# Kernel optimization log

Measured on AMD Instinct MI355X. Metric: run time of the kernel, lower is better.

## Reference

```python
import jax, jax.numpy as jnp
import numpy as np

F = 128
E = 100000   # num_edges
T = 1000000  # num_triplets


def setup_inputs() -> dict:
    key = jax.random.key(0)
    ks = jax.random.split(key, 20)
    s = 0.05
    return {
        "f": jax.random.normal(ks[0], (E, 2 * F), jnp.float32),
        "M01": jax.random.normal(ks[1], (T, F), jnp.float32),
        "M02": jax.random.normal(ks[2], (T, F), jnp.float32),
        # split_net MLP([2F, 2F, 2F]): Linear -> act -> Linear
        "W1": jax.random.normal(ks[3], (2 * F, 2 * F), jnp.float32) * s,
        "b1": jnp.zeros((2 * F,), jnp.float32),
        "W2": jax.random.normal(ks[4], (2 * F, 2 * F), jnp.float32) * s,
        "b2": jnp.zeros((2 * F,), jnp.float32),
        "Ws01": jax.random.normal(ks[5], (F, F), jnp.float32) * s,
        "bs01": jnp.zeros((F,), jnp.float32),
        "Ws02": jax.random.normal(ks[6], (F, F), jnp.float32) * s,
        "bs02": jnp.zeros((F,), jnp.float32),
        "Ws": jax.random.normal(ks[7], (2 * F, F), jnp.float32) * s,
        "bs": jnp.zeros((F,), jnp.float32),
        "Wout": jax.random.normal(ks[8], (F, F), jnp.float32) * s,
        "bout": jnp.zeros((F,), jnp.float32),
        "num_edges": E,
        "idx_ji": jax.random.randint(ks[9], (T,), 0, E, jnp.int32),
        "idx_ki": jax.random.randint(ks[10], (T,), 0, E, jnp.int32),
    }


def reference(f, M01, M02, W1, b1, W2, b2, Ws01, bs01, Ws02, bs02, Ws, bs,
              Wout, bout, num_edges, idx_ji, idx_ki):
    act = jax.nn.silu
    # f = act(split_net(f)); split_net = Linear -> act -> Linear
    h = act(act(f @ W1 + b1) @ W2 + b2)          # [E, 2F]
    f01, f02 = jnp.split(h, 2, axis=-1)           # [E, F] each
    # triplet interaction: gather -> multiply -> linear -> act
    s01 = act((f01[idx_ki] * M01 * f01[idx_ji]) @ Ws01 + bs01)  # [T, F]
    s02 = act((f02[idx_ki] * M02 * f02[idx_ji]) @ Ws02 + bs02)  # [T, F]
    s = act(jnp.concatenate((s01, s02), axis=-1) @ Ws + bs)     # [T, F]
    # scatter-sum triplets back to edges
    out = jax.ops.segment_sum(s, idx_ji, num_segments=num_edges)  # [E, F]
    return out @ Wout + bout
```

## Files before the change

kernel.cpp:

```cpp
#include <hip/hip_runtime.h>

typedef __attribute__((ext_vector_type(8))) short short8;
typedef __attribute__((ext_vector_type(4))) float f32x4;

__device__ __forceinline__ float silu_f(float x) { return x / (1.0f + __expf(-x)); }

__device__ __forceinline__ unsigned short f2bf(float x) {
  unsigned u = __float_as_uint(x);
  u += 0x7FFFu + ((u >> 16) & 1u);
  return (unsigned short)(u >> 16);
}
__device__ __forceinline__ float bf2f(unsigned short v) {
  return __uint_as_float(((unsigned)v) << 16);
}
__device__ __forceinline__ unsigned cvtpk_bf16(float lo, float hi) {
  unsigned r;
  asm("v_cvt_pk_bf16_f32 %0, %1, %2" : "=v"(r) : "v"(lo), "v"(hi));
  return r;
}

#define TSYNC() do { asm volatile("s_waitcnt lgkmcnt(0)" ::: "memory"); \
                     __builtin_amdgcn_s_barrier(); \
                     asm volatile("" ::: "memory"); } while (0)

__global__ void prep_w(const float* __restrict__ W, unsigned short* __restrict__ wh,
                       unsigned short* __restrict__ wl, int K, int N)
{
  int e = blockIdx.x * 256 + threadIdx.x;
  if (e >= K * N) return;
  int k = e / N, n = e % N;
  float w = W[e];
  unsigned short hi = f2bf(w);
  unsigned short lo = f2bf(w - bf2f(hi));
  int kp = k >> 6, kk = k & 63;
  size_t dst = (size_t)kp * N * 64 + (size_t)n * 64 + ((((kk >> 3) ^ (n & 7)) << 3)) + (kk & 7);
  wh[dst] = hi;
  wl[dst] = lo;
}

template<int INBF, int ASPLIT>
__global__ __launch_bounds__(512)
void mlp_gemm(const void* A_, const unsigned short* __restrict__ wh,
              const unsigned short* __restrict__ wl,
              const float* __restrict__ bias, unsigned short* __restrict__ C, int M)
{
  __shared__ unsigned short aTh[64 * 64], aTl[64 * 64];
  __shared__ unsigned short whb[256 * 64], wlb[256 * 64];
  const int tid = threadIdx.x;
  const int lane = tid & 63, wv = tid >> 6;
  const int g = wv & 3, hh = wv >> 2;
  const int l15 = lane & 15, l4 = lane >> 4;
  const int row0 = blockIdx.x * 64;
  const int r = tid >> 3, kseg = (tid & 7) * 8;
  const f32x4 zero4 = {0.f, 0.f, 0.f, 0.f};

  f32x4 acc[8];
#pragma unroll
  for (int nt = 0; nt < 8; nt++) acc[nt] = zero4;

  for (int kp = 0; kp < 4; kp++) {
    {
      const int grow = row0 + r;
      float x[8];
      if (grow < M) {
        if (INBF) {
          short8 v = *(const short8*)((const unsigned short*)A_ + (size_t)grow * 256 + kp * 64 + kseg);
#pragma unroll
          for (int j = 0; j < 8; j++) x[j] = bf2f((unsigned short)v[j]);
        } else {
          const float* ap = (const float*)A_ + (size_t)grow * 256 + kp * 64 + kseg;
          float4 v0 = *(const float4*)ap;
          float4 v1 = *(const float4*)(ap + 4);
          x[0] = v0.x; x[1] = v0.y; x[2] = v0.z; x[3] = v0.w;
          x[4] = v1.x; x[5] = v1.y; x[6] = v1.z; x[7] = v1.w;
        }
      } else {
#pragma unroll
        for (int j = 0; j < 8; j++) x[j] = 0.f;
      }
      union { short8 s; unsigned short us[8]; } H, L;
#pragma unroll
      for (int j = 0; j < 8; j++) {
        H.us[j] = f2bf(x[j]);
        L.us[j] = ASPLIT ? f2bf(x[j] - bf2f(H.us[j])) : (unsigned short)0;
      }
      const int dst = r * 64 + ((((kseg >> 3) ^ (r & 7)) << 3));
      *(short8*)(aTh + dst) = H.s;
      if (ASPLIT) *(short8*)(aTl + dst) = L.s;
    }
    {
      const short8* srcH = (const short8*)(wh + (size_t)kp * 16384);
      const short8* srcL = (const short8*)(wl + (size_t)kp * 16384);
#pragma unroll
      for (int i = 0; i < 4; i++) {
        ((short8*)whb)[tid + 512 * i] = srcH[tid + 512 * i];
        ((short8*)wlb)[tid + 512 * i] = srcL[tid + 512 * i];
      }
    }
    __syncthreads();
#pragma unroll
    for (int ks = 0; ks < 2; ks++) {
      const int arow = 16 * g + l15;
      const int aof = arow * 64 + (((4 * ks + l4) ^ (arow & 7)) << 3);
      short8 ah = *(const short8*)(aTh + aof);
      short8 al = *(const short8*)(aTl + aof);
#pragma unroll
      for (int nt = 0; nt < 8; nt++) {
        const int col = 128 * hh + 16 * nt + l15;
        const int bof = col * 64 + (((4 * ks + l4) ^ (col & 7)) << 3);
        short8 bh = *(const short8*)(whb + bof);
        short8 bl = *(const short8*)(wlb + bof);
        acc[nt] = __builtin_amdgcn_mfma_f32_16x16x32_bf16(ah, bh, acc[nt], 0, 0, 0);
        acc[nt] = __builtin_amdgcn_mfma_f32_16x16x32_bf16(ah, bl, acc[nt], 0, 0, 0);
        if (ASPLIT)
          acc[nt] = __builtin_amdgcn_mfma_f32_16x16x32_bf16(al, bh, acc[nt], 0, 0, 0);
      }
    }
    __syncthreads();
  }
#pragma unroll
  for (int nt = 0; nt < 8; nt++) {
    const int col = 128 * hh + 16 * nt + l15;
    const float bv = bias[col];
#pragma unroll
    for (int i = 0; i < 4; i++) {
      const int row = row0 + 16 * g + 4 * l4 + i;
      if (row < M) C[(size_t)row * 256 + col] = f2bf(silu_f(acc[nt][i] + bv));
    }
  }
}

__global__ __launch_bounds__(512)
void final_gemm(const float* __restrict__ A, const unsigned short* __restrict__ wh,
                const unsigned short* __restrict__ wl,
                const float* __restrict__ bias, float* __restrict__ C, int M)
{
  __shared__ unsigned short aTh[64 * 64], aTl[64 * 64];
  __shared__ unsigned short whb[128 * 64], wlb[128 * 64];
  const int tid = threadIdx.x;
  const int lane = tid & 63, wv = tid >> 6;
  const int g = wv & 3, hh = wv >> 2;
  const int l15 = lane & 15, l4 = lane >> 4;
  const int row0 = blockIdx.x * 64;
  const int r = tid >> 3, kseg = (tid & 7) * 8;
  const f32x4 zero4 = {0.f, 0.f, 0.f, 0.f};

  f32x4 acc[4];
#pragma unroll
  for (int nt = 0; nt < 4; nt++) acc[nt] = zero4;

  for (int kp = 0; kp < 2; kp++) {
    {
      const int grow = row0 + r;
      float x[8];
      if (grow < M) {
        const float* ap = A + (size_t)grow * 128 + kp * 64 + kseg;
        float4 v0 = *(const float4*)ap;
        float4 v1 = *(const float4*)(ap + 4);
        x[0] = v0.x; x[1] = v0.y; x[2] = v0.z; x[3] = v0.w;
        x[4] = v1.x; x[5] = v1.y; x[6] = v1.z; x[7] = v1.w;
      } else {
#pragma unroll
        for (int j = 0; j < 8; j++) x[j] = 0.f;
      }
      union { short8 s; unsigned short us[8]; } H, L;
#pragma unroll
      for (int j = 0; j < 8; j++) {
        H.us[j] = f2bf(x[j]);
        L.us[j] = f2bf(x[j] - bf2f(H.us[j]));
      }
      const int dst = r * 64 + ((((kseg >> 3) ^ (r & 7)) << 3));
      *(short8*)(aTh + dst) = H.s;
      *(short8*)(aTl + dst) = L.s;
    }
    {
      const short8* srcH = (const short8*)(wh + (size_t)kp * 8192);
      const short8* srcL = (const short8*)(wl + (size_t)kp * 8192);
#pragma unroll
      for (int i = 0; i < 2; i++) {
        ((short8*)whb)[tid + 512 * i] = srcH[tid + 512 * i];
        ((short8*)wlb)[tid + 512 * i] = srcL[tid + 512 * i];
      }
    }
    __syncthreads();
#pragma unroll
    for (int ks = 0; ks < 2; ks++) {
      const int arow = 16 * g + l15;
      const int aof = arow * 64 + (((4 * ks + l4) ^ (arow & 7)) << 3);
      short8 ah = *(const short8*)(aTh + aof);
      short8 al = *(const short8*)(aTl + aof);
#pragma unroll
      for (int nt = 0; nt < 4; nt++) {
        const int col = 64 * hh + 16 * nt + l15;
        const int bof = col * 64 + (((4 * ks + l4) ^ (col & 7)) << 3);
        short8 bh = *(const short8*)(whb + bof);
        short8 bl = *(const short8*)(wlb + bof);
        acc[nt] = __builtin_amdgcn_mfma_f32_16x16x32_bf16(ah, bh, acc[nt], 0, 0, 0);
        acc[nt] = __builtin_amdgcn_mfma_f32_16x16x32_bf16(ah, bl, acc[nt], 0, 0, 0);
        acc[nt] = __builtin_amdgcn_mfma_f32_16x16x32_bf16(al, bh, acc[nt], 0, 0, 0);
      }
    }
    __syncthreads();
  }
#pragma unroll
  for (int nt = 0; nt < 4; nt++) {
    const int col = 64 * hh + 16 * nt + l15;
    const float bv = bias[col];
#pragma unroll
    for (int i = 0; i < 4; i++) {
      const int row = row0 + 16 * g + 4 * l4 + i;
      if (row < M) C[(size_t)row * 128 + col] = acc[nt][i] + bv;
    }
  }
}

__global__ void hist_k(const int* __restrict__ ji, int* __restrict__ cnt, int T) {
  int t = blockIdx.x * 256 + threadIdx.x;
  const int stride = gridDim.x * 256;
  for (; t < T; t += stride) atomicAdd(&cnt[ji[t]], 1);
}

__global__ void scan1_k(const int* __restrict__ cnt, int* __restrict__ csum, int E) {
  __shared__ int red[256];
  const int c0 = blockIdx.x * 2048;
  int s = 0;
  for (int i = threadIdx.x; i < 2048; i += 256) {
    int e = c0 + i;
    if (e < E) s += cnt[e];
  }
  red[threadIdx.x] = s;
  __syncthreads();
  for (int o = 128; o > 0; o >>= 1) {
    if (threadIdx.x < o) red[threadIdx.x] += red[threadIdx.x + o];
    __syncthreads();
  }
  if (threadIdx.x == 0) csum[blockIdx.x] = red[0];
}

__global__ void scan2_k(int* __restrict__ csum, int n) {
  if (threadIdx.x == 0 && blockIdx.x == 0) {
    int acc = 0;
    for (int i = 0; i < n; i++) { int v = csum[i]; csum[i] = acc; acc += v; }
  }
}

__global__ void scan3_k(const int* __restrict__ cnt, const int* __restrict__ csum,
                        int* __restrict__ off, int E) {
  __shared__ int ts[256];
  const int c0 = blockIdx.x * 2048;
  const int tid = threadIdx.x;
  int loc[8];
  int s = 0;
#pragma unroll
  for (int k = 0; k < 8; k++) {
    int e = c0 + tid * 8 + k;
    loc[k] = (e < E) ? cnt[e] : 0;
    s += loc[k];
  }
  ts[tid] = s;
  __syncthreads();
  for (int o = 1; o < 256; o <<= 1) {
    int v = (tid >= o) ? ts[tid - o] : 0;
    __syncthreads();
    ts[tid] += v;
    __syncthreads();
  }
  int base = csum[blockIdx.x] + ((tid > 0) ? ts[tid - 1] : 0);
#pragma unroll
  for (int k = 0; k < 8; k++) {
    int e = c0 + tid * 8 + k;
    if (e < E) { off[e] = base; base += loc[k]; }
  }
}

__global__ void scatter_k(const int* __restrict__ ji, int* __restrict__ cursor,
                          int* __restrict__ perm, int T) {
  int t = blockIdx.x * 256 + threadIdx.x;
  const int stride = gridDim.x * 256;
  for (; t < T; t += stride) {
    int e = ji[t];
    int p = atomicAdd(&cursor[e], 1);
    perm[p] = t;
  }
}

struct G12 {
  short8 a0, a1;
  short8 b0, b1;
  float4 m0, m1, m2, m3;
};

__device__ __forceinline__ void issue12(G12& g, const unsigned short* __restrict__ fa,
                                        const unsigned short* __restrict__ fb,
                                        const float* __restrict__ mm, int cseg)
{
  g.a0 = *(const short8*)(fa + cseg);
  g.a1 = *(const short8*)(fa + cseg + 8);
  g.b0 = *(const short8*)(fb + cseg);
  g.b1 = *(const short8*)(fb + cseg + 8);
  g.m0 = *(const float4*)(mm + cseg + 0);
  g.m1 = *(const float4*)(mm + cseg + 4);
  g.m2 = *(const float4*)(mm + cseg + 8);
  g.m3 = *(const float4*)(mm + cseg + 12);
}

__device__ __forceinline__ void pack8x(const short8& a, const short8& b,
                                       const float4& m0, const float4& m1, short8& o)
{
  float p[8];
  p[0] = bf2f((unsigned short)a[0]) * m0.x * bf2f((unsigned short)b[0]);
  p[1] = bf2f((unsigned short)a[1]) * m0.y * bf2f((unsigned short)b[1]);
  p[2] = bf2f((unsigned short)a[2]) * m0.z * bf2f((unsigned short)b[2]);
  p[3] = bf2f((unsigned short)a[3]) * m0.w * bf2f((unsigned short)b[3]);
  p[4] = bf2f((unsigned short)a[4]) * m1.x * bf2f((unsigned short)b[4]);
  p[5] = bf2f((unsigned short)a[5]) * m1.y * bf2f((unsigned short)b[5]);
  p[6] = bf2f((unsigned short)a[6]) * m1.z * bf2f((unsigned short)b[6]);
  p[7] = bf2f((unsigned short)a[7]) * m1.w * bf2f((unsigned short)b[7]);
  union { short8 s; unsigned u[4]; } t;
  t.u[0] = cvtpk_bf16(p[0], p[1]);
  t.u[1] = cvtpk_bf16(p[2], p[3]);
  t.u[2] = cvtpk_bf16(p[4], p[5]);
  t.u[3] = cvtpk_bf16(p[6], p[7]);
  o = t.s;
}

__device__ __forceinline__ void pack16(const G12& g, short8& lo, short8& hi)
{
  pack8x(g.a0, g.b0, g.m0, g.m1, lo);
  pack8x(g.a1, g.b1, g.m2, g.m3, hi);
}

__device__ __forceinline__ void writep(unsigned short* pb, int r, int cseg,
                                       const short8& lo, const short8& hi)
{
  const int c0 = cseg >> 3;
  *(short8*)(pb + r * 128 + (((c0) ^ (r & 7)) << 3)) = lo;
  *(short8*)(pb + r * 128 + (((c0 + 1) ^ (r & 7)) << 3)) = hi;
}

__device__ __forceinline__ void mfma_block4(const unsigned short* abuf,
                                            const unsigned short* wF,
                                            f32x4 (&acc)[4],
                                            int g, int hh, int lane, int l15, int l4)
{
  const int arow = 16 * g + l15;
  __builtin_amdgcn_s_setprio(1);
#pragma unroll
  for (int ks = 0; ks < 4; ks++) {
    short8 a = *(const short8*)(abuf + arow * 128 + (((4 * ks + l4) ^ (arow & 7)) << 3));
#pragma unroll
    for (int ct = 0; ct < 4; ct++) {
      const short8 b = *(const short8*)(wF + (((4 * hh + ct) * 4 + ks) * 64 + lane) * 8);
      acc[ct] = __builtin_amdgcn_mfma_f32_16x16x32_bf16(a, b, acc[ct], 0, 0, 0);
    }
  }
  __builtin_amdgcn_s_setprio(0);
}

__device__ __forceinline__ void store_s(unsigned short* pbuf, const f32x4 (&acc)[4],
                                        const float* __restrict__ bias,
                                        int g, int hh, int l15, int l4)
{
#pragma unroll
  for (int ct = 0; ct < 4; ct++) {
    const int col = 64 * hh + 16 * ct + l15;
    const float bv = bias[col];
#pragma unroll
    for (int i = 0; i < 4; i++) {
      const int r = 16 * g + 4 * l4 + i;
      float v = silu_f(acc[ct][i] + bv);
      pbuf[r * 128 + ((((col >> 3) ^ (r & 7)) << 3)) + (col & 7)] = f2bf(v);
    }
  }
}

__global__ __launch_bounds__(512, 2)
void triplet_fused(const unsigned short* __restrict__ h,
                   const float* __restrict__ M01, const float* __restrict__ M02,
                   const float* __restrict__ Ws01, const float* __restrict__ bs01,
                   const float* __restrict__ Ws02, const float* __restrict__ bs02,
                   const float* __restrict__ Ws,   const float* __restrict__ bs,
                   const int* __restrict__ idx_ji, const int* __restrict__ idx_ki,
                   const int* __restrict__ perm,
                   float* __restrict__ out_acc, int T)
{
  __shared__ unsigned short wF01[16384];
  __shared__ unsigned short wF02[16384];
  __shared__ unsigned short wFA[16384];
  __shared__ unsigned short wFB[16384];
  __shared__ unsigned short pbA[64 * 128];
  __shared__ unsigned short pbB[64 * 128];

  const int tid = threadIdx.x;

  for (int e = tid; e < 16384; e += 512) {
    const int j = e & 7, ln = (e >> 3) & 63, ks = (e >> 9) & 3, ct = e >> 11;
    const int col = 16 * ct + (ln & 15);
    const int k = 32 * ks + 8 * (ln >> 4) + j;
    const int src = k * 128 + col;
    wF01[e] = f2bf(Ws01[src]);
    wF02[e] = f2bf(Ws02[src]);
    wFA[e]  = f2bf(Ws[src]);
    wFB[e]  = f2bf(Ws[16384 + src]);
  }
  __syncthreads();

  const int lane = tid & 63;
  const int wv = tid >> 6;
  const int g = wv & 3;
  const int hh = wv >> 2;
  const int l15 = lane & 15, l4 = lane >> 4;
  const f32x4 zero4 = {0.f, 0.f, 0.f, 0.f};

  float bsv[4];
#pragma unroll
  for (int ct = 0; ct < 4; ct++) bsv[ct] = bs[64 * hh + 16 * ct + l15];

  const int r = tid >> 3;
  const int cseg = (tid & 7) * 16;
  const int ntiles = T >> 6;

  int tile = blockIdx.x;
  if (tile >= ntiles) return;

  int trow = perm[tile * 64 + r];
  int ek = idx_ki[trow], ej = idx_ji[trow];
  short8 p01lo, p01hi;
  {
    G12 g1;
    issue12(g1, h + (size_t)ek * 256, h + (size_t)ej * 256,
            M01 + (size_t)trow * 128, cseg);
    pack16(g1, p01lo, p01hi);
  }

  for (; tile < ntiles; tile += gridDim.x) {
    const int rbase = tile << 6;

    writep(pbA, r, cseg, p01lo, p01hi);
    G12 g2;
    issue12(g2, h + (size_t)ek * 256 + 128, h + (size_t)ej * 256 + 128,
            M02 + (size_t)trow * 128, cseg);
    const int pj = perm[rbase + 16 * g + l15];
    TSYNC();

    int srow_n = (tile + gridDim.x) * 64 + r;
    if (srow_n >= T) srow_n = T - 1;
    const int trow_n = perm[srow_n];
    const int ekn = idx_ki[trow_n], ejn = idx_ji[trow_n];
    const int jrv = idx_ji[pj];
    {
      f32x4 acc1[4] = {zero4, zero4, zero4, zero4};
      mfma_block4(pbA, wF01, acc1, g, hh, lane, l15, l4);
      store_s(pbB, acc1, bs01, g, hh, l15, l4);
    }
    TSYNC();

    f32x4 acc3[4] = {zero4, zero4, zero4, zero4};
    mfma_block4(pbB, wFA, acc3, g, hh, lane, l15, l4);
    {
      short8 lo, hi;
      pack16(g2, lo, hi);
      writep(pbA, r, cseg, lo, hi);
    }
    TSYNC();

    G12 g1n;
    issue12(g1n, h + (size_t)ekn * 256, h + (size_t)ejn * 256,
            M01 + (size_t)trow_n * 128, cseg);
    {
      f32x4 acc2[4] = {zero4, zero4, zero4, zero4};
      mfma_block4(pbA, wF02, acc2, g, hh, lane, l15, l4);
      store_s(pbB, acc2, bs02, g, hh, l15, l4);
    }
    TSYNC();

    mfma_block4(pbB, wFB, acc3, g, hh, lane, l15, l4);
    {
      float sf[4][4];
#pragma unroll
      for (int ct = 0; ct < 4; ct++)
#pragma unroll
        for (int i = 0; i < 4; i++)
          sf[ct][i] = silu_f(acc3[ct][i] + bsv[ct]);

      const int ejp = __shfl_up(jrv, 1, 16);
      unsigned bm = (unsigned)(__ballot((l15 > 0) && (jrv != ejp)) & 0xFFFFull);
      int fr = 0;
      unsigned rem = bm;
      while (fr < 16) {
        const int nxt = rem ? (__ffs(rem) - 1) : 16;
        rem &= rem - 1;
        const int lr = nxt - 1;
        const int e = __shfl(jrv, fr, 16);
        float sv[4];
#pragma unroll
        for (int ct = 0; ct < 4; ct++) {
          float s = 0.f;
#pragma unroll
          for (int i = 0; i < 4; i++) {
            const int rr = 4 * l4 + i;
            s += (rr >= fr && rr <= lr) ? sf[ct][i] : 0.f;
          }
          s += __shfl_xor(s, 16);
          s += __shfl_xor(s, 32);
          sv[ct] = s;
        }
        const float s0 = (l4 == 0) ? sv[0] : (l4 == 1) ? sv[1] : (l4 == 2) ? sv[2] : sv[3];
        float* dst = out_acc + (size_t)e * 128 + 64 * hh + 16 * l4 + l15;
        if (fr == 0 || lr == 15) atomicAdd(dst, s0);
        else *dst = s0;
        fr = nxt;
      }
    }
    pack16(g1n, p01lo, p01hi);
    ek = ekn; ej = ejn; trow = trow_n;
    TSYNC();
  }
}

extern "C" void kernel_launch(void* const* d_in, const int* in_sizes, int n_in,
                              void* d_out, int out_size, void* d_ws, size_t ws_size,
                              hipStream_t stream)
{
  const float* f    = (const float*)d_in[0];
  const float* M01  = (const float*)d_in[1];
  const float* M02  = (const float*)d_in[2];
  const float* W1   = (const float*)d_in[3];
  const float* b1   = (const float*)d_in[4];
  const float* W2   = (const float*)d_in[5];
  const float* b2   = (const float*)d_in[6];
  const float* Ws01 = (const float*)d_in[7];
  const float* bs01 = (const float*)d_in[8];
  const float* Ws02 = (const float*)d_in[9];
  const float* bs02 = (const float*)d_in[10];
  const float* Ws   = (const float*)d_in[11];
  const float* bs   = (const float*)d_in[12];
  const float* Wout = (const float*)d_in[13];
  const float* bout = (const float*)d_in[14];
  const int* idx_ji = (const int*)d_in[16];
  const int* idx_ki = (const int*)d_in[17];

  const int E = in_sizes[0] / 256;
  const int T = in_sizes[1] / 128;

  char* w = (char*)d_ws;
  unsigned short* hbuf = (unsigned short*)w;
  size_t o = ((size_t)E * 256 * 2 + 255) & ~(size_t)255;
  unsigned short* wt1h = (unsigned short*)(w + o); o += 256 * 256 * 2;
  unsigned short* wt1l = (unsigned short*)(w + o); o += 256 * 256 * 2;
  unsigned short* wt2h = (unsigned short*)(w + o); o += 256 * 256 * 2;
  unsigned short* wt2l = (unsigned short*)(w + o); o += 256 * 256 * 2;
  unsigned short* wtoh = (unsigned short*)(w + o); o += 128 * 128 * 2;
  unsigned short* wtol = (unsigned short*)(w + o); o += 128 * 128 * 2;
  o = (o + 255) & ~(size_t)255;
  int* cnt = (int*)(w + o);  o += ((size_t)E * 4 + 255) & ~(size_t)255;
  int* off = (int*)(w + o);  o += ((size_t)E * 4 + 255) & ~(size_t)255;
  int* csum = (int*)(w + o); o += 4096;
  int* perm = (int*)(w + o);

  float* out_acc = (float*)d_out;
  const int mb = (E + 63) / 64;

  prep_w<<<(256 * 256 + 255) / 256, 256, 0, stream>>>(W1, wt1h, wt1l, 256, 256);
  prep_w<<<(256 * 256 + 255) / 256, 256, 0, stream>>>(W2, wt2h, wt2l, 256, 256);
  prep_w<<<(128 * 128 + 255) / 256, 256, 0, stream>>>(Wout, wtoh, wtol, 128, 128);

  mlp_gemm<0, 1><<<mb, 512, 0, stream>>>(f, wt1h, wt1l, b1, hbuf, E);
  mlp_gemm<1, 0><<<mb, 512, 0, stream>>>(hbuf, wt2h, wt2l, b2, hbuf, E);

  hipMemsetAsync(cnt, 0, (size_t)E * 4, stream);
  hist_k<<<1024, 256, 0, stream>>>(idx_ji, cnt, T);
  const int nchunks = (E + 2047) / 2048;
  scan1_k<<<nchunks, 256, 0, stream>>>(cnt, csum, E);
  scan2_k<<<1, 64, 0, stream>>>(csum, nchunks);
  scan3_k<<<nchunks, 256, 0, stream>>>(cnt, csum, off, E);
  scatter_k<<<1024, 256, 0, stream>>>(idx_ji, off, perm, T);

  hipMemsetAsync(d_out, 0, (size_t)E * 128 * sizeof(float), stream);

  const int ntiles = (T + 63) / 64;
  const int grid = ntiles < 256 ? ntiles : 256;
  triplet_fused<<<grid, 512, 0, stream>>>(hbuf, M01, M02, Ws01, bs01, Ws02, bs02,
                                          Ws, bs, idx_ji, idx_ki, perm, out_acc, T);

  final_gemm<<<mb, 512, 0, stream>>>(out_acc, wtoh, wtol, bout, out_acc, E);
}
```

Measured before the change: 962.2 us.

## Deepen triplet gather prefetch pipeline and merge weight prep kernels

The fused triplet kernel now prefetches M01 gathers two tiles ahead using double-buffered register sets, issues the M02 gather for the next tile one phase earlier, and loads indices three tiles ahead. The goal is to hide more of the latency of the random gathers behind the MFMA work. The three weight-prep launches are also merged into one kernel to save launch overhead. The deeper prefetch holds more live registers, which risks spills or lower occupancy, and it leaves a dead prologue gather whose result is discarded.

```diff
diff --git a/kernel.cpp b/kernel.cpp
--- a/kernel.cpp
+++ b/kernel.cpp
@@ -23,11 +23,11 @@
                      __builtin_amdgcn_s_barrier(); \
                      asm volatile("" ::: "memory"); } while (0)
 
-__global__ void prep_w(const float* __restrict__ W, unsigned short* __restrict__ wh,
-                       unsigned short* __restrict__ wl, int K, int N)
-{
-  int e = blockIdx.x * 256 + threadIdx.x;
-  if (e >= K * N) return;
+__device__ __forceinline__ void prep_one(const float* __restrict__ W,
+                                         unsigned short* __restrict__ wh,
+                                         unsigned short* __restrict__ wl,
+                                         int N, int e)
+{
   int k = e / N, n = e % N;
   float w = W[e];
   unsigned short hi = f2bf(w);
@@ -36,6 +36,18 @@
   size_t dst = (size_t)kp * N * 64 + (size_t)n * 64 + ((((kk >> 3) ^ (n & 7)) << 3)) + (kk & 7);
   wh[dst] = hi;
   wl[dst] = lo;
+}
+
+__global__ void prep_all(const float* __restrict__ W1, unsigned short* w1h, unsigned short* w1l,
+                         const float* __restrict__ W2, unsigned short* w2h, unsigned short* w2l,
+                         const float* __restrict__ Wo, unsigned short* woh, unsigned short* wol)
+{
+  int e = blockIdx.x * 256 + threadIdx.x;
+  if (e < 256 * 256) {
+    prep_one(W1, w1h, w1l, 256, e);
+    prep_one(W2, w2h, w2l, 256, e);
+  }
+  if (e < 128 * 128) prep_one(Wo, woh, wol, 128, e);
 }
 
 template<int INBF, int ASPLIT>
@@ -419,34 +431,50 @@
   const int r = tid >> 3;
   const int cseg = (tid & 7) * 16;
   const int ntiles = T >> 6;
+  const int G = gridDim.x;
 
   int tile = blockIdx.x;
   if (tile >= ntiles) return;
 
-  int trow = perm[tile * 64 + r];
-  int ek = idx_ki[trow], ej = idx_ji[trow];
+  auto srow = [&](int q) { int s = q * 64 + r; return s < T ? s : T - 1; };
+
+  int trow1, trow2, trow3;
+  int ek1, ej1, ek2, ej2;
+  {
+    const int trow0 = perm[srow(tile)];
+    trow1 = perm[srow(tile + G)];
+    trow2 = perm[srow(tile + 2 * G)];
+    const int ek0 = idx_ki[trow0], ej0 = idx_ji[trow0];
+    ek1 = idx_ki[trow1]; ej1 = idx_ji[trow1];
+    ek2 = idx_ki[trow2]; ej2 = idx_ji[trow2];
+
+    G12 gP;
+    issue12(gP, h + (size_t)ek0 * 256, h + (size_t)ej0 * 256, M01 + (size_t)trow0 * 128, cseg);
+    trow3 = trow0;
+    (void)gP;
+    short8 tmplo, tmphi;
+    (void)tmplo; (void)tmphi;
+  }
+
+  G12 gA, gB, g2;
   short8 p01lo, p01hi;
   {
-    G12 g1;
-    issue12(g1, h + (size_t)ek * 256, h + (size_t)ej * 256,
-            M01 + (size_t)trow * 128, cseg);
-    pack16(g1, p01lo, p01hi);
-  }
-
-  for (; tile < ntiles; tile += gridDim.x) {
-    const int rbase = tile << 6;
-
+    const int trow0 = perm[srow(tile)];
+    const int ek0 = idx_ki[trow0], ej0 = idx_ji[trow0];
+    issue12(gA, h + (size_t)ek0 * 256, h + (size_t)ej0 * 256, M01 + (size_t)trow0 * 128, cseg);
+    issue12(gB, h + (size_t)ek1 * 256, h + (size_t)ej1 * 256, M01 + (size_t)trow1 * 128, cseg);
+    issue12(g2, h + (size_t)ek0 * 256 + 128, h + (size_t)ej0 * 256 + 128,
+            M02 + (size_t)trow0 * 128, cseg);
+    pack16(gA, p01lo, p01hi);
+  }
+  int parity = 0;
+
+  for (; tile < ntiles; tile += G) {
     writep(pbA, r, cseg, p01lo, p01hi);
-    G12 g2;
-    issue12(g2, h + (size_t)ek * 256 + 128, h + (size_t)ej * 256 + 128,
-            M02 + (size_t)trow * 128, cseg);
-    const int pj = perm[rbase + 16 * g + l15];
+    const int pj = perm[(tile << 6) + 16 * g + l15];
     TSYNC();
 
-    int srow_n = (tile + gridDim.x) * 64 + r;
-    if (srow_n >= T) srow_n = T - 1;
-    const int trow_n = perm[srow_n];
-    const int ekn = idx_ki[trow_n], ejn = idx_ji[trow_n];
+    trow3 = perm[srow(tile + 3 * G)];
     const int jrv = idx_ji[pj];
     {
       f32x4 acc1[4] = {zero4, zero4, zero4, zero4};
@@ -462,11 +490,14 @@
       pack16(g2, lo, hi);
       writep(pbA, r, cseg, lo, hi);
     }
+    issue12(g2, h + (size_t)ek1 * 256 + 128, h + (size_t)ej1 * 256 + 128,
+            M02 + (size_t)trow1 * 128, cseg);
     TSYNC();
 
-    G12 g1n;
-    issue12(g1n, h + (size_t)ekn * 256, h + (size_t)ejn * 256,
-            M01 + (size_t)trow_n * 128, cseg);
+    if (parity == 0)
+      issue12(gA, h + (size_t)ek2 * 256, h + (size_t)ej2 * 256, M01 + (size_t)trow2 * 128, cseg);
+    else
+      issue12(gB, h + (size_t)ek2 * 256, h + (size_t)ej2 * 256, M01 + (size_t)trow2 * 128, cseg);
     {
       f32x4 acc2[4] = {zero4, zero4, zero4, zero4};
       mfma_block4(pbA, wF02, acc2, g, hh, lane, l15, l4);
@@ -475,6 +506,7 @@
     TSYNC();
 
     mfma_block4(pbB, wFB, acc3, g, hh, lane, l15, l4);
+    const int ek3 = idx_ki[trow3], ej3 = idx_ji[trow3];
     {
       float sf[4][4];
 #pragma unroll
@@ -512,8 +544,11 @@
         fr = nxt;
       }
     }
-    pack16(g1n, p01lo, p01hi);
-    ek = ekn; ej = ejn; trow = trow_n;
+    if (parity == 0) pack16(gB, p01lo, p01hi);
+    else             pack16(gA, p01lo, p01hi);
+    parity ^= 1;
+    ek1 = ek2; ej1 = ej2; trow1 = trow2;
+    ek2 = ek3; ej2 = ej3; trow2 = trow3;
     TSYNC();
   }
 }
@@ -561,9 +596,9 @@
   float* out_acc = (float*)d_out;
   const int mb = (E + 63) / 64;
 
-  prep_w<<<(256 * 256 + 255) / 256, 256, 0, stream>>>(W1, wt1h, wt1l, 256, 256);
-  prep_w<<<(256 * 256 + 255) / 256, 256, 0, stream>>>(W2, wt2h, wt2l, 256, 256);
-  prep_w<<<(128 * 128 + 255) / 256, 256, 0, stream>>>(Wout, wtoh, wtol, 128, 128);
+  prep_all<<<(256 * 256 + 255) / 256, 256, 0, stream>>>(W1, wt1h, wt1l,
+                                                        W2, wt2h, wt2l,
+                                                        Wout, wtoh, wtol);
 
   mlp_gemm<0, 1><<<mb, 512, 0, stream>>>(f, wt1h, wt1l, b1, hbuf, E);
   mlp_gemm<1, 0><<<mb, 512, 0, stream>>>(hbuf, wt2h, wt2l, b2, hbuf, E);
```

Measured after the change: 940.8 us. -2.2%, faster.
